# Kernel optimization log

Hardware: AMD Instinct MI355X
Metric: run time of the kernel (lower is better)

The kernel has to match this reference:

```python
import jax, jax.numpy as jnp
import numpy as np
import math

EMBED_DIM = 1024
N_HEAD = 16
HEAD_DIM = EMBED_DIM // N_HEAD


def setup_inputs() -> dict:
    key = jax.random.key(0)
    ks = jax.random.split(key, 9)
    B, T, C = 4, 2048, EMBED_DIM
    s = 1.0 / math.sqrt(C)
    return {
        "x": jax.random.normal(ks[0], (B, T, C), dtype=jnp.float32),
        "Wq": jax.random.normal(ks[1], (C, C), dtype=jnp.float32) * s,
        "bq": jnp.zeros((C,), dtype=jnp.float32),
        "Wk": jax.random.normal(ks[2], (C, C), dtype=jnp.float32) * s,
        "bk": jnp.zeros((C,), dtype=jnp.float32),
        "Wv": jax.random.normal(ks[3], (C, C), dtype=jnp.float32) * s,
        "bv": jnp.zeros((C,), dtype=jnp.float32),
        "Wp": jax.random.normal(ks[4], (C, C), dtype=jnp.float32) * s,
        "bp": jnp.zeros((C,), dtype=jnp.float32),
    }


def reference(x, Wq, bq, Wk, bk, Wv, bv, Wp, bp):
    B, T, C = x.shape
    H, D = N_HEAD, HEAD_DIM

    def heads(W, b):
        # [B,T,C] -> [B,H,T,D]
        return (x @ W.T + b).reshape(B, T, H, D).transpose(0, 2, 1, 3)

    q = heads(Wq, bq)
    k = heads(Wk, bk)
    v = heads(Wv, bv)

    att = jnp.einsum("bhtd,bhsd->bhts", q, k) * (1.0 / math.sqrt(D))
    causal = jnp.tril(jnp.ones((T, T), dtype=bool))
    att = jnp.where(causal[None, None], att, -jnp.inf)
    att = jax.nn.softmax(att, axis=-1)
    y = jnp.einsum("bhts,bhsd->bhtd", att, v)  # [B,H,T,D]
    y = y.transpose(0, 2, 1, 3).reshape(B, T, C)
    return y @ Wp.T + bp
```

## Files before the change

### kernel.cpp

```cpp
#include <hip/hip_runtime.h>
#include <hip/hip_bf16.h>
#include <cstdint>
#include <cstddef>

#define TQ 2048
#define CDIM 1024
#define NH 16
#define HD 64

typedef __attribute__((ext_vector_type(8))) short bf16x8;
typedef __attribute__((ext_vector_type(4))) float f32x4;
typedef __attribute__((ext_vector_type(16))) float f32x16;

__device__ __forceinline__ unsigned short f2bf(float f) {
  union { float f; unsigned u; } x; x.f = f;
  unsigned r = x.u + 0x7fffu + ((x.u >> 16) & 1u);
  return (unsigned short)(r >> 16);
}

__device__ __forceinline__ unsigned cvtpk(float lo, float hi) {
  unsigned r;
  asm("v_cvt_pk_bf16_f32 %0, %1, %2" : "=v"(r) : "v"(lo), "v"(hi));
  return r;
}

__device__ __forceinline__ void plswap(unsigned& x, unsigned& y) {
  asm("v_permlane32_swap_b32 %0, %1" : "+v"(x), "+v"(y));
}

__device__ __forceinline__ float exp2_fast(float x) {
  float r;
  asm("v_exp_f32 %0, %1" : "=v"(r) : "v"(x));
  return r;
}

__device__ __forceinline__ void gload_lds16(const void* g, void* l) {
  typedef __attribute__((address_space(1))) const void gv;
  typedef __attribute__((address_space(3))) void lv;
  __builtin_amdgcn_global_load_lds((gv*)g, (lv*)l, 16, 0, 0);
}

__global__ void cvt_bf16_kernel(const float* __restrict__ in,
                                unsigned short* __restrict__ out, int n) {
  int stride = gridDim.x * blockDim.x;
  for (int i = blockIdx.x * blockDim.x + threadIdx.x; i * 4 < n; i += stride) {
    float4 v = *(const float4*)(in + (size_t)i * 4);
    ushort4 o;
    o.x = f2bf(v.x); o.y = f2bf(v.y); o.z = f2bf(v.z); o.w = f2bf(v.w);
    *(ushort4*)(out + (size_t)i * 4) = o;
  }
}

__global__ void cvt4_kernel(const float* __restrict__ w0, const float* __restrict__ w1,
                            const float* __restrict__ w2, const float* __restrict__ w3,
                            unsigned short* __restrict__ out) {
  int i = blockIdx.x * blockDim.x + threadIdx.x;
  int which = i >> 18;
  const float* src = which == 0 ? w0 : which == 1 ? w1 : which == 2 ? w2 : w3;
  int off = (i & 262143) * 4;
  float4 v = *(const float4*)(src + off);
  ushort4 o;
  o.x = f2bf(v.x); o.y = f2bf(v.y); o.z = f2bf(v.z); o.w = f2bf(v.w);
  *(ushort4*)(out + (size_t)i * 4) = o;
}

template <int EPI>
__global__ __launch_bounds__(256) void gemm_bt_kernel(
    const unsigned short* __restrict__ A,
    const unsigned short* __restrict__ Bt,
    const float* __restrict__ b0, const float* __restrict__ b1,
    void* __restrict__ outp,
    int M, int N, int K) {
  __shared__ __align__(16) unsigned short As[128 * 64];
  __shared__ __align__(16) unsigned short Bs[128 * 64];

  const int nbm = M >> 7;
  const int nbn = N >> 7;
  const int nwg = nbm * nbn;
  int id = (int)blockIdx.x;
  const int cpx = nwg >> 3;
  id = (id & 7) * cpx + (id >> 3);
  const int tm = id % nbm;
  const int tn = id / nbm;

  const int tid = threadIdx.x;
  const int w = tid >> 6, lane = tid & 63;
  const int g = lane >> 4, c = lane & 15;
  const int wr = w >> 1, wc = w & 1;

  const unsigned short* Ab = A + (size_t)tm * 128 * K;
  const unsigned short* Bb = Bt + (size_t)tn * 128 * K;
  const int Kb = K * 2;

  f32x4 acc[4][4];
#pragma unroll
  for (int i = 0; i < 4; ++i)
#pragma unroll
    for (int j = 0; j < 4; ++j) acc[i][j] = (f32x4){0.f, 0.f, 0.f, 0.f};

  for (int kt = 0; kt < K; kt += 64) {
#pragma unroll
    for (int i = 0; i < 4; ++i) {
      const int seg = w * 4 + i;
      const int off = seg * 1024 + lane * 16;
      const int row = off >> 7;
      const int colB = off & 127;
      gload_lds16((const char*)Ab + (size_t)row * Kb + kt * 2 + colB,
                  (char*)As + seg * 1024);
      gload_lds16((const char*)Bb + (size_t)row * Kb + kt * 2 + colB,
                  (char*)Bs + seg * 1024);
    }
    __syncthreads();
#pragma unroll
    for (int ki = 0; ki < 2; ++ki) {
      bf16x8 af[4], bv[4];
#pragma unroll
      for (int mi = 0; mi < 4; ++mi)
        af[mi] = *(const bf16x8*)(As + (wr * 64 + mi * 16 + c) * 64 + ki * 32 + g * 8);
#pragma unroll
      for (int ni = 0; ni < 4; ++ni)
        bv[ni] = *(const bf16x8*)(Bs + (wc * 64 + ni * 16 + c) * 64 + ki * 32 + g * 8);
#pragma unroll
      for (int mi = 0; mi < 4; ++mi)
#pragma unroll
        for (int ni = 0; ni < 4; ++ni)
          acc[mi][ni] = __builtin_amdgcn_mfma_f32_16x16x32_bf16(
              af[mi], bv[ni], acc[mi][ni], 0, 0, 0);
    }
    __syncthreads();
  }

#pragma unroll
  for (int mi = 0; mi < 4; ++mi) {
#pragma unroll
    for (int ni = 0; ni < 4; ++ni) {
      const int n = tn * 128 + wc * 64 + ni * 16 + c;
#pragma unroll
      for (int e = 0; e < 4; ++e) {
        const int m = tm * 128 + wr * 64 + mi * 16 + g * 4 + e;
        float v = acc[mi][ni][e];
        if (EPI == 1) {
          v += b0[m];
          size_t idx = ((size_t)(n >> 11) * (NH * HD) + m) * TQ + (n & (TQ - 1));
          ((unsigned short*)outp)[idx] = f2bf(v);
        } else if (EPI == 2) {
          v += b0[n];
          ((float*)outp)[(size_t)m * N + n] = v;
        } else {
          unsigned short* O = (unsigned short*)outp;
          if (n < 1024) {
            v = (v + b0[n]) * 0.18033688f;
            size_t idx = ((size_t)(m >> 11) * NH + (n >> 6)) * (TQ * HD) +
                         (size_t)(m & (TQ - 1)) * HD + (n & (HD - 1));
            O[idx] = f2bf(v);
          } else {
            int nn = n - 1024;
            v += b1[nn];
            size_t idx = 8388608 + ((size_t)(m >> 11) * NH + (nn >> 6)) * (TQ * HD) +
                         (size_t)(m & (TQ - 1)) * HD + (nn & (HD - 1));
            O[idx] = f2bf(v);
          }
        }
      }
    }
  }
}

__global__ __launch_bounds__(256, 4) void attn_kernel(
    const unsigned short* __restrict__ Q,
    const unsigned short* __restrict__ K,
    const unsigned short* __restrict__ Vt,
    unsigned short* __restrict__ Y) {
  __shared__ __align__(16) char Ks[2][8192];
  __shared__ __align__(16) char Vs[2][8192];

  const int tid = (int)threadIdx.x;
  const int w = tid >> 6, lane = tid & 63;
  const int l31 = lane & 31, hi = lane >> 5;

  const int n = (int)blockIdx.x;
  const int g = n & 255, k = n >> 8;
  const int bh = g >> 2;
  const int u = 2 * (g & 3) + (k >> 1);
  const int qt = (k & 1) ? (15 - u) : u;
  const int b = bh >> 4, h = bh & 15;

  const unsigned short* Qb = Q + (size_t)bh * TQ * HD;
  const char* Kb = (const char*)(K + (size_t)bh * TQ * HD);
  const char* Vb = (const char*)(Vt + (size_t)bh * HD * TQ);

  auto stage = [&](int buf, int kt) {
#pragma unroll
    for (int i = 0; i < 2; ++i) {
      const int s = i * 256 + tid;
      const int r32 = (s >> 8) * 32 + (s & 31);
      const int ck = ((s >> 6) & 3) * 32 + ((s >> 5) & 1) * 16;
      char* kdst = &Ks[buf][0] + i * 4096 + (w << 10);
      char* vdst = &Vs[buf][0] + i * 4096 + (w << 10);
      gload_lds16(Kb + (size_t)kt * 8192 + r32 * 128 + ck, kdst);
      gload_lds16(Vb + (size_t)r32 * 4096 + kt * 128 + ck, vdst);
    }
  };

  const int q0 = qt * 128 + w * 32;
  const int qg = q0 + l31;
  const int nkv = 2 * qt + 2;

  stage(0, 0);

  bf16x8 qf[4];
#pragma unroll
  for (int dk = 0; dk < 4; ++dk)
    qf[dk] = *(const bf16x8*)(Qb + (size_t)qg * HD + dk * 16 + hi * 8);

  f32x16 oac[2];
#pragma unroll
  for (int nb = 0; nb < 2; ++nb)
#pragma unroll
    for (int r = 0; r < 16; ++r) oac[nb][r] = 0.f;
  float mr = -3.0e38f, lr = 0.f;

  __syncthreads();

  for (int kt = 0; kt < nkv; ++kt) {
    const int cur = kt & 1;
    if (kt + 1 < nkv) stage(cur ^ 1, kt + 1);

    if (kt * 64 <= q0 + 31) {
      const char* Klane = &Ks[cur][0] + lane * 16;
      const char* Vlane = &Vs[cur][0] + lane * 16;

      f32x16 s0, s1;
#pragma unroll
      for (int r = 0; r < 16; ++r) { s0[r] = 0.f; s1[r] = 0.f; }
#pragma unroll
      for (int dk = 0; dk < 4; ++dk) {
        bf16x8 kf0 = *(const bf16x8*)(Klane + (dk << 10));
        bf16x8 kf1 = *(const bf16x8*)(Klane + ((4 + dk) << 10));
        s0 = __builtin_amdgcn_mfma_f32_32x32x16_bf16(kf0, qf[dk], s0, 0, 0, 0);
        s1 = __builtin_amdgcn_mfma_f32_32x32x16_bf16(kf1, qf[dk], s1, 0, 0, 0);
      }

      const bool maskT = (kt * 64 + 63 > q0);
      if (maskT) {
#pragma unroll
        for (int r = 0; r < 16; ++r) {
          int kv0 = kt * 64 + ((r & 3) + 8 * (r >> 2)) + 4 * hi;
          s0[r] = (kv0 <= qg) ? s0[r] : -3.0e38f;
          s1[r] = (kv0 + 32 <= qg) ? s1[r] : -3.0e38f;
        }
      }

      float mt_ = s0[0];
#pragma unroll
      for (int r = 1; r < 16; ++r) mt_ = fmaxf(mt_, s0[r]);
#pragma unroll
      for (int r = 0; r < 16; ++r) mt_ = fmaxf(mt_, s1[r]);
      mt_ = fmaxf(mt_, __shfl_xor(mt_, 32));

      if (!__all(mt_ - mr <= 8.0f)) {
        const float mn = fmaxf(mr, mt_);
        const float al = exp2_fast(mr - mn);
        mr = mn;
        lr *= al;
#pragma unroll
        for (int nb = 0; nb < 2; ++nb)
#pragma unroll
          for (int r = 0; r < 16; ++r) oac[nb][r] *= al;
      }

      float rs = 0.f;
#pragma unroll
      for (int r = 0; r < 16; ++r) { s0[r] = exp2_fast(s0[r] - mr); rs += s0[r]; }
#pragma unroll
      for (int r = 0; r < 16; ++r) { s1[r] = exp2_fast(s1[r] - mr); rs += s1[r]; }
      rs += __shfl_xor(rs, 32);
      lr += rs;

      bf16x8 pf[4];
      {
        unsigned a0 = cvtpk(s0[0], s0[1]), b0 = cvtpk(s0[2], s0[3]);
        unsigned c0 = cvtpk(s0[4], s0[5]), d0 = cvtpk(s0[6], s0[7]);
        plswap(a0, c0); plswap(b0, d0);
        unsigned a1 = cvtpk(s0[8], s0[9]), b1 = cvtpk(s0[10], s0[11]);
        unsigned c1 = cvtpk(s0[12], s0[13]), d1 = cvtpk(s0[14], s0[15]);
        plswap(a1, c1); plswap(b1, d1);
        unsigned a2 = cvtpk(s1[0], s1[1]), b2 = cvtpk(s1[2], s1[3]);
        unsigned c2 = cvtpk(s1[4], s1[5]), d2 = cvtpk(s1[6], s1[7]);
        plswap(a2, c2); plswap(b2, d2);
        unsigned a3 = cvtpk(s1[8], s1[9]), b3 = cvtpk(s1[10], s1[11]);
        unsigned c3 = cvtpk(s1[12], s1[13]), d3 = cvtpk(s1[14], s1[15]);
        plswap(a3, c3); plswap(b3, d3);
        union { unsigned u[4]; bf16x8 v; } t;
        t.u[0] = a0; t.u[1] = b0; t.u[2] = c0; t.u[3] = d0; pf[0] = t.v;
        t.u[0] = a1; t.u[1] = b1; t.u[2] = c1; t.u[3] = d1; pf[1] = t.v;
        t.u[0] = a2; t.u[1] = b2; t.u[2] = c2; t.u[3] = d2; pf[2] = t.v;
        t.u[0] = a3; t.u[1] = b3; t.u[2] = c3; t.u[3] = d3; pf[3] = t.v;
      }

#pragma unroll
      for (int nb = 0; nb < 2; ++nb)
#pragma unroll
        for (int ks = 0; ks < 4; ++ks) {
          bf16x8 vf = *(const bf16x8*)(Vlane + (((nb << 2) + ks) << 10));
          oac[nb] = __builtin_amdgcn_mfma_f32_32x32x16_bf16(vf, pf[ks], oac[nb], 0, 0, 0);
        }
    }
    __syncthreads();
  }

  float inv;
  asm("v_rcp_f32 %0, %1" : "=v"(inv) : "v"(lr));
  unsigned short* Yrow = Y + (size_t)(b * TQ + qg) * CDIM + h * 64;
#pragma unroll
  for (int nb = 0; nb < 2; ++nb)
#pragma unroll
    for (int j = 0; j < 8; ++j) {
      const int dbase = ((2 * j) & 3) + 8 * (j >> 1);
      unsigned lo = f2bf(oac[nb][2 * j] * inv);
      unsigned hi2 = f2bf(oac[nb][2 * j + 1] * inv);
      *(unsigned*)(Yrow + nb * 32 + dbase + 4 * hi) = lo | (hi2 << 16);
    }
}

extern "C" void kernel_launch(void* const* d_in, const int* in_sizes, int n_in,
                              void* d_out, int out_size, void* d_ws, size_t ws_size,
                              hipStream_t stream) {
  (void)in_sizes; (void)n_in; (void)out_size; (void)ws_size;
  const float* x  = (const float*)d_in[0];
  const float* Wq = (const float*)d_in[1];
  const float* bq = (const float*)d_in[2];
  const float* Wk = (const float*)d_in[3];
  const float* bk = (const float*)d_in[4];
  const float* Wv = (const float*)d_in[5];
  const float* bv = (const float*)d_in[6];
  const float* Wp = (const float*)d_in[7];
  const float* bp = (const float*)d_in[8];
  float* out = (float*)d_out;

  char* ws = (char*)d_ws;
  unsigned short* xb  = (unsigned short*)(ws + 0);
  unsigned short* wqb = (unsigned short*)(ws + 16777216);
  unsigned short* wvb = (unsigned short*)(ws + 20971520);
  unsigned short* wpb = (unsigned short*)(ws + 23068672);
  unsigned short* Qh  = (unsigned short*)(ws + 25165824);
  unsigned short* Kh  = (unsigned short*)(ws + 41943040);
  unsigned short* Vt  = (unsigned short*)(ws + 58720256);
  unsigned short* y   = (unsigned short*)(ws + 75497472);

  const int nx = 4 * TQ * CDIM;

  cvt_bf16_kernel<<<4096, 256, 0, stream>>>(x, xb, nx);
  cvt4_kernel<<<4096, 256, 0, stream>>>(Wq, Wk, Wv, Wp, wqb);

  gemm_bt_kernel<4><<<1024, 256, 0, stream>>>(xb, wqb, bq, bk, Qh, 8192, 2048, 1024);
  gemm_bt_kernel<1><<<512, 256, 0, stream>>>(wvb, xb, bv, bv, Vt, 1024, 8192, 1024);

  attn_kernel<<<1024, 256, 0, stream>>>(Qh, Kh, Vt, y);

  gemm_bt_kernel<2><<<512, 256, 0, stream>>>(y, wpb, bp, bp, out, 8192, 1024, 1024);
}
```

Before: 212.9 us.

## Replace 128x128 GEMM with double-buffered 256x256 8-wave pipelined GEMM

Replaces the 128x128-tile, 4-wave GEMM with a 256x256-tile, 8-wave kernel. It double-buffers K-slices in 128 KB of LDS and interleaves global->LDS staging of half-tiles with LDS reads and MFMA subtiles, using explicit vmcnt waits, barriers and s_setprio. This aims to raise arithmetic intensity and hide load latency behind compute. The trade-off is that grids shrink to 128-256 workgroups on a 256-CU device, so some CUs sit idle and the tail is poor. The 128 KB LDS footprint also allows only one block per CU.

```diff
diff --git a/kernel.cpp b/kernel.cpp
--- a/kernel.cpp
+++ b/kernel.cpp
@@ -39,6 +39,10 @@
   typedef __attribute__((address_space(3))) void lv;
   __builtin_amdgcn_global_load_lds((gv*)g, (lv*)l, 16, 0, 0);
 }
+
+#define BAR() do { asm volatile("" ::: "memory"); __builtin_amdgcn_s_barrier(); asm volatile("" ::: "memory"); } while (0)
+#define VMC2() asm volatile("s_waitcnt vmcnt(2)" ::: "memory")
+#define VMC0() asm volatile("s_waitcnt vmcnt(0)" ::: "memory")
 
 __global__ void cvt_bf16_kernel(const float* __restrict__ in,
                                 unsigned short* __restrict__ out, int n) {
@@ -65,79 +69,115 @@
 }
 
 template <int EPI>
-__global__ __launch_bounds__(256) void gemm_bt_kernel(
+__global__ __launch_bounds__(512, 2) void gemm256_kernel(
     const unsigned short* __restrict__ A,
     const unsigned short* __restrict__ Bt,
     const float* __restrict__ b0, const float* __restrict__ b1,
     void* __restrict__ outp,
     int M, int N, int K) {
-  __shared__ __align__(16) unsigned short As[128 * 64];
-  __shared__ __align__(16) unsigned short Bs[128 * 64];
-
-  const int nbm = M >> 7;
-  const int nbn = N >> 7;
+  __shared__ __align__(16) char lds[131072];
+
+  const int tid = (int)threadIdx.x;
+  const int w = tid >> 6, lane = tid & 63;
+  const int g = lane >> 4, c = lane & 15;
+  const int wm = w >> 2, wn = w & 3;
+
+  const int nbm = M >> 8, nbn = N >> 8;
   const int nwg = nbm * nbn;
   int id = (int)blockIdx.x;
   const int cpx = nwg >> 3;
   id = (id & 7) * cpx + (id >> 3);
-  const int tm = id % nbm;
-  const int tn = id / nbm;
-
-  const int tid = threadIdx.x;
-  const int w = tid >> 6, lane = tid & 63;
-  const int g = lane >> 4, c = lane & 15;
-  const int wr = w >> 1, wc = w & 1;
-
-  const unsigned short* Ab = A + (size_t)tm * 128 * K;
-  const unsigned short* Bb = Bt + (size_t)tn * 128 * K;
-  const int Kb = K * 2;
-
-  f32x4 acc[4][4];
-#pragma unroll
-  for (int i = 0; i < 4; ++i)
+  const int tm = id % nbm, tn = id / nbm;
+
+  const char* Ab = (const char*)(A + (size_t)tm * 256 * K);
+  const char* Bb = (const char*)(Bt + (size_t)tn * 256 * K);
+  const int rowB = K * 2;
+  const int nht = (K >> 6) << 2;
+
+  char* aw = lds + wm * 16384;
+  char* bw = lds + 65536 + (wn >> 1) * 16384;
+  const int bfo = (wn & 1) * 8;
+
+  auto stage_ht = [&](int j) {
+    if (j >= nht) return;
+    const int t = j >> 2, part = j & 3;
+    const int isB = part >> 1, half = part & 1;
+    const char* src = isB ? Bb : Ab;
+    char* dst = lds + isB * 65536 + (t & 1) * 32768 + half * 16384 + w * 2048;
+#pragma unroll
+    for (int r = 0; r < 2; ++r) {
+      const int f = w * 2 + r;
+      const int m16 = f >> 1, ki = f & 1;
+      gload_lds16(src + (size_t)(half * 128 + m16 * 16 + c) * rowB +
+                      t * 128 + ki * 64 + g * 16,
+                  dst + r * 1024);
+    }
+  };
+
+  f32x4 acc[8][4];
+#pragma unroll
+  for (int i = 0; i < 8; ++i)
 #pragma unroll
     for (int j = 0; j < 4; ++j) acc[i][j] = (f32x4){0.f, 0.f, 0.f, 0.f};
-
-  for (int kt = 0; kt < K; kt += 64) {
-#pragma unroll
-    for (int i = 0; i < 4; ++i) {
-      const int seg = w * 4 + i;
-      const int off = seg * 1024 + lane * 16;
-      const int row = off >> 7;
-      const int colB = off & 127;
-      gload_lds16((const char*)Ab + (size_t)row * Kb + kt * 2 + colB,
-                  (char*)As + seg * 1024);
-      gload_lds16((const char*)Bb + (size_t)row * Kb + kt * 2 + colB,
-                  (char*)Bs + seg * 1024);
-    }
-    __syncthreads();
-#pragma unroll
-    for (int ki = 0; ki < 2; ++ki) {
-      bf16x8 af[4], bv[4];
-#pragma unroll
-      for (int mi = 0; mi < 4; ++mi)
-        af[mi] = *(const bf16x8*)(As + (wr * 64 + mi * 16 + c) * 64 + ki * 32 + g * 8);
-#pragma unroll
-      for (int ni = 0; ni < 4; ++ni)
-        bv[ni] = *(const bf16x8*)(Bs + (wc * 64 + ni * 16 + c) * 64 + ki * 32 + g * 8);
-#pragma unroll
-      for (int mi = 0; mi < 4; ++mi)
-#pragma unroll
-        for (int ni = 0; ni < 4; ++ni)
-          acc[mi][ni] = __builtin_amdgcn_mfma_f32_16x16x32_bf16(
-              af[mi], bv[ni], acc[mi][ni], 0, 0, 0);
-    }
-    __syncthreads();
+  bf16x8 af[4][2], bv[2][2];
+
+  auto rdA = [&](int buf, int ms) {
+#pragma unroll
+    for (int mi = 0; mi < 4; ++mi)
+#pragma unroll
+      for (int ki = 0; ki < 2; ++ki)
+        af[mi][ki] = *(const bf16x8*)(aw + buf * 32768 +
+                                      ((ms * 4 + mi) * 2 + ki) * 1024 + lane * 16);
+  };
+  auto rdB = [&](int buf, int ns) {
+#pragma unroll
+    for (int ni = 0; ni < 2; ++ni)
+#pragma unroll
+      for (int ki = 0; ki < 2; ++ki)
+        bv[ni][ki] = *(const bf16x8*)(bw + buf * 32768 +
+                                      (bfo + (ns * 2 + ni) * 2 + ki) * 1024 + lane * 16);
+  };
+  auto mm = [&](int ms, int ns) {
+    __builtin_amdgcn_s_setprio(1);
+#pragma unroll
+    for (int mi = 0; mi < 4; ++mi)
+#pragma unroll
+      for (int ni = 0; ni < 2; ++ni)
+#pragma unroll
+        for (int ki = 0; ki < 2; ++ki)
+          acc[ms * 4 + mi][ns * 2 + ni] = __builtin_amdgcn_mfma_f32_16x16x32_bf16(
+              af[mi][ki], bv[ni][ki], acc[ms * 4 + mi][ns * 2 + ni], 0, 0, 0);
+    __builtin_amdgcn_s_setprio(0);
+  };
+
+  for (int j = 0; j < 5; ++j) stage_ht(j);
+  VMC2();
+  BAR();
+
+  const int niter = K >> 7;
+#pragma unroll 1
+  for (int i = 0; i < niter; ++i) {
+    const int j0 = 5 + (i << 3);
+    rdA(0, 0); rdB(0, 0); stage_ht(j0 + 0); BAR(); mm(0, 0); BAR();
+    rdB(0, 1);            stage_ht(j0 + 1); BAR(); mm(0, 1); BAR();
+    rdA(0, 1);            stage_ht(j0 + 2); BAR(); mm(1, 1); BAR();
+    rdB(0, 0);            stage_ht(j0 + 3);
+    if (i + 1 < niter) { VMC2(); } else { VMC0(); }
+    BAR(); mm(1, 0); BAR();
+    rdA(1, 0); rdB(1, 0); stage_ht(j0 + 4); BAR(); mm(0, 0); BAR();
+    rdB(1, 1);            stage_ht(j0 + 5); BAR(); mm(0, 1); BAR();
+    rdA(1, 1);            stage_ht(j0 + 6); BAR(); mm(1, 1); BAR();
+    rdB(1, 0);            stage_ht(j0 + 7); VMC2(); BAR(); mm(1, 0); BAR();
   }
 
 #pragma unroll
-  for (int mi = 0; mi < 4; ++mi) {
+  for (int mi = 0; mi < 8; ++mi) {
 #pragma unroll
     for (int ni = 0; ni < 4; ++ni) {
-      const int n = tn * 128 + wc * 64 + ni * 16 + c;
+      const int n = tn * 256 + wn * 64 + ni * 16 + c;
 #pragma unroll
       for (int e = 0; e < 4; ++e) {
-        const int m = tm * 128 + wr * 64 + mi * 16 + g * 4 + e;
+        const int m = tm * 256 + wm * 128 + mi * 16 + g * 4 + e;
         float v = acc[mi][ni][e];
         if (EPI == 1) {
           v += b0[m];
@@ -353,10 +393,10 @@
   cvt_bf16_kernel<<<4096, 256, 0, stream>>>(x, xb, nx);
   cvt4_kernel<<<4096, 256, 0, stream>>>(Wq, Wk, Wv, Wp, wqb);
 
-  gemm_bt_kernel<4><<<1024, 256, 0, stream>>>(xb, wqb, bq, bk, Qh, 8192, 2048, 1024);
-  gemm_bt_kernel<1><<<512, 256, 0, stream>>>(wvb, xb, bv, bv, Vt, 1024, 8192, 1024);
+  gemm256_kernel<4><<<256, 512, 0, stream>>>(xb, wqb, bq, bk, Qh, 8192, 2048, 1024);
+  gemm256_kernel<1><<<128, 512, 0, stream>>>(wvb, xb, bv, bv, Vt, 1024, 8192, 1024);
 
   attn_kernel<<<1024, 256, 0, stream>>>(Qh, Kh, Vt, y);
 
-  gemm_bt_kernel<2><<<512, 256, 0, stream>>>(y, wpb, bp, bp, out, 8192, 1024, 1024);
-}
+  gemm256_kernel<2><<<128, 512, 0, stream>>>(y, wpb, bp, bp, out, 8192, 1024, 1024);
+}
```

Result: slower. 218.3 us (+2.5%).
